# Performance work log

Measured on AMD Instinct MI355X. Metric: run time of the kernel, lower is better.

The kernel has to match this reference:

```python
import jax, jax.numpy as jnp
import numpy as np

N_ITEMS = 2000
N_STORAGE = 4094
N_LOCS = N_STORAGE + 2  # storage locations + start + end
E = 4_194_304
HID = 32


def setup_inputs() -> dict:
    rng = np.random.default_rng(0)
    etype = rng.integers(0, 3, size=E)  # 0: loc-loc, 1: item-item, 2: item-loc
    src = np.empty(E, dtype=np.int64)
    dst = np.empty(E, dtype=np.int64)
    m0, m1, m2 = (etype == 0), (etype == 1), (etype == 2)
    src[m0] = rng.integers(N_ITEMS, N_ITEMS + N_LOCS, m0.sum())
    dst[m0] = rng.integers(N_ITEMS, N_ITEMS + N_LOCS, m0.sum())
    src[m1] = rng.integers(0, N_ITEMS, m1.sum())
    dst[m1] = rng.integers(0, N_ITEMS, m1.sum())
    src[m2] = rng.integers(0, N_ITEMS, m2.sum())
    dst[m2] = rng.integers(N_ITEMS, N_ITEMS + N_STORAGE, m2.sum())
    edge_index = jnp.asarray(np.stack([src, dst]))
    edge_attr = jnp.asarray(rng.random((E, 2)).astype(np.float32))
    edge_type_mask = jnp.asarray(np.eye(3, dtype=bool)[etype])
    k1, k2 = jax.random.split(jax.random.key(0))
    W1 = jax.random.normal(k1, (3, HID), jnp.float32) * 0.5
    b1 = jnp.zeros((HID,), jnp.float32)
    W2 = jax.random.normal(k2, (HID, 1), jnp.float32) * 0.5
    b2 = jnp.zeros((1,), jnp.float32)
    return {
        "edge_index": edge_index,
        "edge_attr": edge_attr,
        "edge_type_mask": edge_type_mask,
        "n_items": N_ITEMS,
        "n_storage": N_STORAGE,
        "n_locs": N_LOCS,
        "W1": W1, "b1": b1, "W2": W2, "b2": b2,
    }


def reference(edge_index, edge_attr, edge_type_mask, n_items, n_storage, n_locs,
              W1, b1, W2, b2):
    src, dst = edge_index[0], edge_index[1]

    # --- loc-loc distance matrix: scatter masked edges into [n_locs, n_locs] ---
    ls, ld = src - n_items, dst - n_items
    v = edge_type_mask[:, 0] & (ls >= 0) & (ls < n_locs) & (ld >= 0) & (ld < n_locs)
    ls = jnp.where(v, ls, n_locs)  # invalid -> out of bounds, dropped by scatter
    ld = jnp.where(v, ld, n_locs)
    loc_mat = jnp.zeros((n_locs, n_locs), edge_attr.dtype).at[ls, ld].set(
        edge_attr[:, 0], mode="drop")

    # --- item-item sequence-count matrix: [n_items, n_items] ---
    v = edge_type_mask[:, 1] & (src >= 0) & (src < n_items) & (dst >= 0) & (dst < n_items)
    is_ = jnp.where(v, src, n_items)
    id_ = jnp.where(v, dst, n_items)
    seq_mat = jnp.zeros((n_items, n_items), edge_attr.dtype).at[is_, id_].set(
        edge_attr[:, 1], mode="drop")

    # --- item -> storage-location assignment: [n_items] int ---
    li = dst - n_items
    v = edge_type_mask[:, 2] & (src >= 0) & (src < n_items) & (li >= 0) & (li < n_storage)
    ii = jnp.where(v, src, n_items)
    item_to_loc = jnp.zeros((n_items,), jnp.int32).at[ii].set(
        jnp.where(v, li, 0).astype(jnp.int32), mode="drop")

    # --- item_item_dist = sum_{i,j: seq>0} seq_mat[i,j] * loc_mat[loc_i, loc_j] ---
    gathered = loc_mat[item_to_loc][:, item_to_loc]  # [n_items, n_items]
    item_item_dist = jnp.sum(jnp.where(seq_mat > 0, seq_mat * gathered, 0.0))

    # --- start / end depot distances (start_idx = n_storage, end_idx = n_storage+1) ---
    start_dist = jnp.sum(loc_mat[n_storage, item_to_loc]) if n_storage < n_locs else jnp.float32(0.0)
    end_dist = jnp.sum(loc_mat[item_to_loc, n_storage + 1]) if n_storage + 1 < n_locs else jnp.float32(0.0)

    comps = jnp.stack([item_item_dist, start_dist, end_dist])[None, :]  # [1, 3]
    h = jax.nn.relu(comps @ W1 + b1)
    pred = h @ W2 + b2  # [1, 1]
    return pred.squeeze()
```

## Files before the change

kernel.cpp:

```cpp
#include <hip/hip_runtime.h>

#define N_ITEMS   2000
#define N_STORAGE 4094
#define N_LOCS    4096
#define E_EDGES   4194304
#define LOCD      2048
#define NBLKB     512
#define BCAP      8192
#define SGRP      500
#define LGRP      512
#define NG        1012
#define NROWS     1013

typedef unsigned int u32;
typedef int vi4 __attribute__((ext_vector_type(4)));

__device__ __forceinline__ int wave_incl_scan(int v) {
    #pragma unroll
    for (int o = 1; o < 64; o <<= 1) {
        int u = __shfl_up(v, o);
        if ((threadIdx.x & 63) >= o) v += u;
    }
    return v;
}

__global__ __launch_bounds__(1024)
void bin_all(const int* __restrict__ src, const int* __restrict__ dst,
             u32* __restrict__ recbuf, int* __restrict__ pfx,
             int* __restrict__ slab, int* __restrict__ flags4) {
    __shared__ int lwin[N_ITEMS];
    __shared__ int cnt[NG];
    __shared__ int excl[NG];
    __shared__ int wsum[16];
    int t = threadIdx.x;
    for (int i = t; i < N_ITEMS; i += 1024) lwin[i] = -1;
    for (int i = t; i < NG; i += 1024) cnt[i] = 0;
    if (t < 32) flags4[blockIdx.x * 32 + t] = 0;
    int rel0 = t * 8;
    int base = blockIdx.x * BCAP + rel0;
    vi4 sa = __builtin_nontemporal_load((const vi4*)&src[base]);
    vi4 sb = __builtin_nontemporal_load((const vi4*)&src[base + 4]);
    vi4 da = __builtin_nontemporal_load((const vi4*)&dst[base]);
    vi4 db = __builtin_nontemporal_load((const vi4*)&dst[base + 4]);
    __syncthreads();
    int ss[8] = {sa[0], sa[1], sa[2], sa[3], sb[0], sb[1], sb[2], sb[3]};
    int dd[8] = {da[0], da[1], da[2], da[3], db[0], db[1], db[2], db[3]};
    u32 meta[8], ilcol[8];
    #pragma unroll
    for (int k = 0; k < 8; ++k) {
        int s = ss[k], d = dd[k];
        u32 m = 0xFFFFFFFFu, ic = 0;
        if ((unsigned)s < N_ITEMS) {
            if ((unsigned)d < N_ITEMS) {
                int g = s >> 2;
                m = ((u32)atomicAdd(&cnt[g], 1) << 10) | (u32)g;
                ic = ((u32)(s & 3) << 25) | ((u32)d << 13);
            } else {
                unsigned li = (unsigned)(d - N_ITEMS);
                if (li < N_STORAGE) atomicMax(&lwin[s], base + k);
            }
        } else {
            unsigned ls = (unsigned)(s - N_ITEMS), ld = (unsigned)(d - N_ITEMS);
            if (ls < N_LOCS && ld < N_LOCS) {
                int g = SGRP + (int)(ls >> 3);
                m = ((u32)atomicAdd(&cnt[g], 1) << 10) | (u32)g;
                ic = ((ls & 7u) << 25) | (ld << 13);
            }
        }
        meta[k] = m;
        ilcol[k] = ic;
    }
    __syncthreads();
    int v = (t < NG) ? cnt[t] : 0;
    int inc = wave_incl_scan(v);
    if ((t & 63) == 63) wsum[t >> 6] = inc;
    __syncthreads();
    int w = t >> 6, woff = 0;
    #pragma unroll
    for (int k = 0; k < 16; ++k) woff += (k < w) ? wsum[k] : 0;
    int ex = inc - v + woff;
    if (t < NG) {
        excl[t] = ex;
        pfx[t * NBLKB + blockIdx.x] = ex;
    }
    if (t == 0) {
        int tot = 0;
        #pragma unroll
        for (int k = 0; k < 16; ++k) tot += wsum[k];
        pfx[NG * NBLKB + blockIdx.x] = tot;
    }
    __syncthreads();
    u32* rb = recbuf + (size_t)blockIdx.x * BCAP;
    #pragma unroll
    for (int k = 0; k < 8; ++k) {
        u32 m = meta[k];
        if (m != 0xFFFFFFFFu) {
            int g = (int)(m & 1023u), rank = (int)(m >> 10);
            rb[excl[g] + rank] = ilcol[k] | (u32)(rel0 + k);
        }
    }
    for (int i = t; i < N_ITEMS; i += 1024) slab[blockIdx.x * 2048 + i] = lwin[i];
}

__global__ __launch_bounds__(1024)
void item_reduce(const int* __restrict__ slab, const int* __restrict__ dst,
                 int* __restrict__ item_loc, int* __restrict__ used_row,
                 int* __restrict__ used_col) {
    __shared__ int red[16][64];
    int t = threadIdx.x;
    int lane = t & 63, sub = t >> 6;
    int i = blockIdx.x * 64 + lane;
    int m = -1;
    for (int b = sub; b < NBLKB; b += 16)
        m = max(m, slab[b * 2048 + i]);
    red[sub][lane] = m;
    __syncthreads();
    if (sub == 0 && i < N_ITEMS) {
        #pragma unroll
        for (int k = 1; k < 16; ++k) m = max(m, red[k][lane]);
        int loc = (m >= 0) ? (dst[m] - N_ITEMS) : 0;
        item_loc[i] = loc;
        used_row[loc] = 1;
        used_col[loc] = 1;
    }
    if (blockIdx.x == 0 && t == 0) {
        used_row[N_STORAGE] = 1;
        used_col[N_STORAGE + 1] = 1;
    }
}

__global__ __launch_bounds__(1024)
void remap_fused(const int* __restrict__ used_row, const int* __restrict__ used_col,
                 const int* __restrict__ item_loc, int* __restrict__ rrow,
                 int* __restrict__ rcol, int* __restrict__ item_rr,
                 int* __restrict__ item_rc, int* __restrict__ rse) {
    __shared__ int wsA[16], wsB[16];
    int t = threadIdx.x;
    vi4 ur = *(const vi4*)&used_row[t * 4];
    vi4 uc = *(const vi4*)&used_col[t * 4];
    int sA = ur[0] + ur[1] + ur[2] + ur[3];
    int sB = uc[0] + uc[1] + uc[2] + uc[3];
    int iA = wave_incl_scan(sA);
    int iB = wave_incl_scan(sB);
    if ((t & 63) == 63) { wsA[t >> 6] = iA; wsB[t >> 6] = iB; }
    __syncthreads();
    int w = t >> 6, oA = 0, oB = 0;
    #pragma unroll
    for (int k = 0; k < 16; ++k) {
        oA += (k < w) ? wsA[k] : 0;
        oB += (k < w) ? wsB[k] : 0;
    }
    int runA = iA - sA + oA;
    int runB = iB - sB + oB;
    vi4 rr4, rc4;
    #pragma unroll
    for (int j = 0; j < 4; ++j) {
        runA += ur[j]; rr4[j] = ur[j] ? runA : 0;
        runB += uc[j]; rc4[j] = uc[j] ? runB : 0;
    }
    *(vi4*)&rrow[t * 4] = rr4;
    *(vi4*)&rcol[t * 4] = rc4;
    __syncthreads();
    for (int i = t; i < N_ITEMS; i += 1024) {
        int loc = item_loc[i];
        item_rr[i] = rrow[loc] - 1;
        item_rc[i] = rcol[loc] - 1;
    }
    if (t == 0) {
        rse[0] = rrow[N_STORAGE] - 1;
        rse[1] = rcol[N_STORAGE + 1] - 1;
    }
}

__global__ __launch_bounds__(1024)
void loc_dedup(const u32* __restrict__ recbuf, const int* __restrict__ pfx,
               const float* __restrict__ attr, const int* __restrict__ rrow,
               const int* __restrict__ rcol, float* __restrict__ locf) {
    __shared__ u32 win[8 * 2048];
    __shared__ short rcol_s[N_LOCS];
    __shared__ int rrow8[8];
    int t = threadIdx.x, g = blockIdx.x;
    if (t < 8) rrow8[t] = rrow[g * 8 + t];
    for (int i = t; i < 8 * 2048; i += 1024) win[i] = 0;
    for (int i = t; i < N_LOCS; i += 1024) rcol_s[i] = (short)rcol[i];
    __syncthreads();
    int row = SGRP + g;
    int b = t >> 1, half = t & 1;
    int s0 = pfx[row * NBLKB + b], s1 = pfx[(row + 1) * NBLKB + b];
    const u32* rb = recbuf + (size_t)b * BCAP;
    u32 kb = ((u32)b << 13) + 1;
    for (int r = s0 + half; r < s1; r += 2) {
        u32 rec = rb[r];
        int il = (int)(rec >> 25);
        if (rrow8[il] <= 0) continue;
        int rc = rcol_s[(rec >> 13) & 4095u];
        if (rc <= 0) continue;
        atomicMax(&win[il * 2048 + rc - 1], kb + (rec & 8191u));
    }
    __syncthreads();
    for (int il = 0; il < 8; ++il) {
        int cr = rrow8[il];
        if (cr <= 0) continue;
        const u32* wrow = &win[il * 2048];
        float* orow = locf + (size_t)(cr - 1) * LOCD;
        for (int i = t; i < 2048; i += 1024) {
            u32 w = wrow[i];
            orow[i] = w ? attr[2 * (int)(w - 1)] : 0.f;
        }
    }
}

__global__ __launch_bounds__(1024)
void seq_dedup(const u32* __restrict__ recbuf, const int* __restrict__ pfx,
               const float* __restrict__ attr, const float* __restrict__ locf,
               const int* __restrict__ item_rr, const int* __restrict__ item_rc,
               const int* __restrict__ rse, float* __restrict__ gpart) {
    __shared__ u32 win[4 * 2048];
    __shared__ short rcs[N_ITEMS];
    __shared__ int rrs[4];
    __shared__ float red[16][3];
    int t = threadIdx.x, g = blockIdx.x;
    for (int i = t; i < 4 * 2048; i += 1024) win[i] = 0;
    for (int i = t; i < N_ITEMS; i += 1024) rcs[i] = (short)item_rc[i];
    if (t < 4) rrs[t] = item_rr[g * 4 + t];
    __syncthreads();
    int b = t >> 1, half = t & 1;
    int s0 = pfx[g * NBLKB + b], s1 = pfx[(g + 1) * NBLKB + b];
    const u32* rb = recbuf + (size_t)b * BCAP;
    u32 kb = ((u32)b << 13) + 1;
    for (int r = s0 + half; r < s1; r += 2) {
        u32 rec = rb[r];
        int slot = (((int)(rec >> 25) & 3) << 11) | (int)((rec >> 13) & 2047u);
        atomicMax(&win[slot], kb + (rec & 8191u));
    }
    __syncthreads();
    float acc = 0.f, sd = 0.f, ed = 0.f;
    for (int i = t; i < 4 * 2048; i += 1024) {
        u32 w = win[i];
        if (w) {
            float seq = attr[2 * (int)(w - 1) + 1];
            if (seq > 0.f)
                acc += seq * locf[(size_t)rrs[i >> 11] * LOCD + (int)rcs[i & 2047]];
        }
    }
    if (t < 4) {
        sd = locf[(size_t)rse[0] * LOCD + (int)rcs[g * 4 + t]];
        ed = locf[(size_t)rrs[t] * LOCD + rse[1]];
    }
    #pragma unroll
    for (int o = 32; o > 0; o >>= 1) {
        acc += __shfl_down(acc, o);
        sd  += __shfl_down(sd, o);
        ed  += __shfl_down(ed, o);
    }
    if ((t & 63) == 0) { red[t >> 6][0] = acc; red[t >> 6][1] = sd; red[t >> 6][2] = ed; }
    __syncthreads();
    if (t == 0) {
        float a = 0.f, bb = 0.f, c = 0.f;
        #pragma unroll
        for (int k = 0; k < 16; ++k) { a += red[k][0]; bb += red[k][1]; c += red[k][2]; }
        gpart[g * 3 + 0] = a;
        gpart[g * 3 + 1] = bb;
        gpart[g * 3 + 2] = c;
    }
}

__global__ void final_mlp(const float* __restrict__ gpart, const float* __restrict__ W1,
                          const float* __restrict__ b1, const float* __restrict__ W2,
                          const float* __restrict__ b2, float* __restrict__ out) {
    __shared__ float s0[4], s1[4], s2[4];
    int t = threadIdx.x;
    float a = 0.f, b = 0.f, c = 0.f;
    for (int i = t; i < SGRP; i += 256) {
        a += gpart[i * 3 + 0];
        b += gpart[i * 3 + 1];
        c += gpart[i * 3 + 2];
    }
    #pragma unroll
    for (int o = 32; o > 0; o >>= 1) {
        a += __shfl_down(a, o);
        b += __shfl_down(b, o);
        c += __shfl_down(c, o);
    }
    if ((t & 63) == 0) { s0[t >> 6] = a; s1[t >> 6] = b; s2[t >> 6] = c; }
    __syncthreads();
    float v = 0.f;
    if (t < 32) {
        float ca = s0[0] + s0[1] + s0[2] + s0[3];
        float cb = s1[0] + s1[1] + s1[2] + s1[3];
        float cc = s2[0] + s2[1] + s2[2] + s2[3];
        float h = ca * W1[t] + cb * W1[32 + t] + cc * W1[64 + t] + b1[t];
        h = fmaxf(h, 0.f);
        v = h * W2[t];
    }
    #pragma unroll
    for (int o = 32; o > 0; o >>= 1) v += __shfl_down(v, o);
    if (t == 0) out[0] = v + b2[0];
}

extern "C" void kernel_launch(void* const* d_in, const int* in_sizes, int n_in,
                              void* d_out, int out_size, void* d_ws, size_t ws_size,
                              hipStream_t stream) {
    const int*   eidx = (const int*)d_in[0];
    const int*   src  = eidx;
    const int*   dst  = eidx + E_EDGES;
    const float* attr = (const float*)d_in[1];
    const float* W1 = (const float*)d_in[6];
    const float* b1 = (const float*)d_in[7];
    const float* W2 = (const float*)d_in[8];
    const float* b2 = (const float*)d_in[9];

    u32*   recbuf   = (u32*)d_ws;
    float* locf     = (float*)(recbuf + (size_t)NBLKB * BCAP);
    int*   used_row = (int*)(locf + (size_t)LOCD * LOCD);
    int*   used_col = used_row + N_LOCS;
    int*   rrow     = used_col + N_LOCS;
    int*   rcol     = rrow + N_LOCS;
    int*   pfx      = rcol + N_LOCS;
    int*   slab     = pfx + NROWS * NBLKB;
    int*   item_loc = slab + NBLKB * 2048;
    int*   item_rr  = item_loc + N_ITEMS;
    int*   item_rc  = item_rr + N_ITEMS;
    int*   rse      = item_rc + N_ITEMS;
    float* gpart    = (float*)(rse + 2);

    bin_all    <<<NBLKB, 1024, 0, stream>>>(src, dst, recbuf, pfx, slab, used_row);
    item_reduce<<<32, 1024, 0, stream>>>(slab, dst, item_loc, used_row, used_col);
    remap_fused<<<1, 1024, 0, stream>>>(used_row, used_col, item_loc, rrow, rcol,
                                        item_rr, item_rc, rse);
    loc_dedup  <<<LGRP, 1024, 0, stream>>>(recbuf, pfx, attr, rrow, rcol, locf);
    seq_dedup  <<<SGRP, 1024, 0, stream>>>(recbuf, pfx, attr, locf,
                                           item_rr, item_rc, rse, gpart);
    final_mlp  <<<1, 256, 0, stream>>>(gpart, W1, b1, W2, b2, (float*)d_out);
}
```

Before: 88.52 us.

## Halve binning blocks and carry seq attribute inside 64-bit records

The binning kernel now runs 256 blocks of 16384 edges each and streams the edge attributes alongside src/dst. Item-item records become 64-bit values that carry the seq float, so seq_dedup does its atomicMax on 64-bit keys and no longer gathers attr at random. Seq and loc records go to separate buffers with their own prefix arrays, and the dedup kernels use 4 threads per source block instead of 2. In exchange, bin_all reads every attribute and has fewer blocks, which lowers its parallelism, and the 64-bit LDS atomics and larger record buffers add cost.

```diff
diff --git a/kernel.cpp b/kernel.cpp
--- a/kernel.cpp
+++ b/kernel.cpp
@@ -5,15 +5,16 @@
 #define N_LOCS    4096
 #define E_EDGES   4194304
 #define LOCD      2048
-#define NBLKB     512
-#define BCAP      8192
+#define NBLKB     256
+#define BCAP      16384
 #define SGRP      500
 #define LGRP      512
 #define NG        1012
-#define NROWS     1013
-
+
+typedef unsigned long long u64;
 typedef unsigned int u32;
-typedef int vi4 __attribute__((ext_vector_type(4)));
+typedef int   vi4 __attribute__((ext_vector_type(4)));
+typedef float vf4 __attribute__((ext_vector_type(4)));
 
 __device__ __forceinline__ int wave_incl_scan(int v) {
     #pragma unroll
@@ -26,77 +27,99 @@
 
 __global__ __launch_bounds__(1024)
 void bin_all(const int* __restrict__ src, const int* __restrict__ dst,
-             u32* __restrict__ recbuf, int* __restrict__ pfx,
+             const float* __restrict__ attr, u64* __restrict__ seqrec,
+             u32* __restrict__ locrec, int* __restrict__ pfxS, int* __restrict__ pfxL,
              int* __restrict__ slab, int* __restrict__ flags4) {
     __shared__ int lwin[N_ITEMS];
     __shared__ int cnt[NG];
-    __shared__ int excl[NG];
+    __shared__ int exclS[SGRP];
+    __shared__ int exclL[LGRP];
     __shared__ int wsum[16];
     int t = threadIdx.x;
     for (int i = t; i < N_ITEMS; i += 1024) lwin[i] = -1;
     for (int i = t; i < NG; i += 1024) cnt[i] = 0;
-    if (t < 32) flags4[blockIdx.x * 32 + t] = 0;
-    int rel0 = t * 8;
-    int base = blockIdx.x * BCAP + rel0;
-    vi4 sa = __builtin_nontemporal_load((const vi4*)&src[base]);
-    vi4 sb = __builtin_nontemporal_load((const vi4*)&src[base + 4]);
-    vi4 da = __builtin_nontemporal_load((const vi4*)&dst[base]);
-    vi4 db = __builtin_nontemporal_load((const vi4*)&dst[base + 4]);
-    __syncthreads();
-    int ss[8] = {sa[0], sa[1], sa[2], sa[3], sb[0], sb[1], sb[2], sb[3]};
-    int dd[8] = {da[0], da[1], da[2], da[3], db[0], db[1], db[2], db[3]};
-    u32 meta[8], ilcol[8];
-    #pragma unroll
-    for (int k = 0; k < 8; ++k) {
-        int s = ss[k], d = dd[k];
-        u32 m = 0xFFFFFFFFu, ic = 0;
-        if ((unsigned)s < N_ITEMS) {
-            if ((unsigned)d < N_ITEMS) {
-                int g = s >> 2;
-                m = ((u32)atomicAdd(&cnt[g], 1) << 10) | (u32)g;
-                ic = ((u32)(s & 3) << 25) | ((u32)d << 13);
+    if (t < 64) flags4[blockIdx.x * 64 + t] = 0;
+    __syncthreads();
+
+    u32 meta[16], aux[16], val[16];
+    #pragma unroll
+    for (int r = 0; r < 2; ++r) {
+        int rel0 = r * 8192 + t * 8;
+        int base = blockIdx.x * BCAP + rel0;
+        vi4 sa = __builtin_nontemporal_load((const vi4*)&src[base]);
+        vi4 sb = __builtin_nontemporal_load((const vi4*)&src[base + 4]);
+        vi4 da = __builtin_nontemporal_load((const vi4*)&dst[base]);
+        vi4 db = __builtin_nontemporal_load((const vi4*)&dst[base + 4]);
+        vf4 a0 = __builtin_nontemporal_load((const vf4*)&attr[base * 2]);
+        vf4 a1 = __builtin_nontemporal_load((const vf4*)&attr[base * 2 + 4]);
+        vf4 a2 = __builtin_nontemporal_load((const vf4*)&attr[base * 2 + 8]);
+        vf4 a3 = __builtin_nontemporal_load((const vf4*)&attr[base * 2 + 12]);
+        int ss[8] = {sa[0], sa[1], sa[2], sa[3], sb[0], sb[1], sb[2], sb[3]};
+        int dd[8] = {da[0], da[1], da[2], da[3], db[0], db[1], db[2], db[3]};
+        float v1[8] = {a0[1], a0[3], a1[1], a1[3], a2[1], a2[3], a3[1], a3[3]};
+        #pragma unroll
+        for (int k = 0; k < 8; ++k) {
+            int e = r * 8 + k;
+            int s = ss[k], d = dd[k];
+            u32 m = 0xFFFFFFFFu, ic = 0, vv = 0;
+            if ((unsigned)s < N_ITEMS) {
+                if ((unsigned)d < N_ITEMS) {
+                    int g = s >> 2;
+                    m = ((u32)atomicAdd(&cnt[g], 1) << 10) | (u32)g;
+                    ic = ((u32)(s & 3) << 25) | ((u32)d << 14) | (u32)(rel0 + k);
+                    vv = __float_as_uint(v1[k]);
+                } else {
+                    unsigned li = (unsigned)(d - N_ITEMS);
+                    if (li < N_STORAGE) atomicMax(&lwin[s], base + k);
+                }
             } else {
-                unsigned li = (unsigned)(d - N_ITEMS);
-                if (li < N_STORAGE) atomicMax(&lwin[s], base + k);
+                unsigned ls = (unsigned)(s - N_ITEMS), ld = (unsigned)(d - N_ITEMS);
+                if (ls < N_LOCS && ld < N_LOCS) {
+                    int g = SGRP + (int)(ls >> 3);
+                    m = ((u32)atomicAdd(&cnt[g], 1) << 10) | (u32)g;
+                    ic = ((ls & 7u) << 26) | (ld << 14) | (u32)(rel0 + k);
+                }
             }
-        } else {
-            unsigned ls = (unsigned)(s - N_ITEMS), ld = (unsigned)(d - N_ITEMS);
-            if (ls < N_LOCS && ld < N_LOCS) {
-                int g = SGRP + (int)(ls >> 3);
-                m = ((u32)atomicAdd(&cnt[g], 1) << 10) | (u32)g;
-                ic = ((ls & 7u) << 25) | (ld << 13);
-            }
+            meta[e] = m;
+            aux[e] = ic;
+            val[e] = vv;
         }
-        meta[k] = m;
-        ilcol[k] = ic;
-    }
-    __syncthreads();
-    int v = (t < NG) ? cnt[t] : 0;
+    }
+    __syncthreads();
+    int v;
+    if (t < 512) v = (t < SGRP) ? cnt[t] : 0;
+    else         v = cnt[t - 12];
     int inc = wave_incl_scan(v);
     if ((t & 63) == 63) wsum[t >> 6] = inc;
     __syncthreads();
-    int w = t >> 6, woff = 0;
-    #pragma unroll
-    for (int k = 0; k < 16; ++k) woff += (k < w) ? wsum[k] : 0;
+    int w = t >> 6, lo = (t < 512) ? 0 : 8, woff = 0;
+    #pragma unroll
+    for (int k = 0; k < 16; ++k) woff += (k >= lo && k < w) ? wsum[k] : 0;
     int ex = inc - v + woff;
-    if (t < NG) {
-        excl[t] = ex;
-        pfx[t * NBLKB + blockIdx.x] = ex;
+    if (t < SGRP) {
+        exclS[t] = ex;
+        pfxS[t * NBLKB + blockIdx.x] = ex;
+    } else if (t >= 512) {
+        exclL[t - 512] = ex;
+        pfxL[(t - 512) * NBLKB + blockIdx.x] = ex;
     }
     if (t == 0) {
-        int tot = 0;
+        int t0 = 0, t1 = 0;
         #pragma unroll
-        for (int k = 0; k < 16; ++k) tot += wsum[k];
-        pfx[NG * NBLKB + blockIdx.x] = tot;
-    }
-    __syncthreads();
-    u32* rb = recbuf + (size_t)blockIdx.x * BCAP;
-    #pragma unroll
-    for (int k = 0; k < 8; ++k) {
-        u32 m = meta[k];
+        for (int k = 0; k < 8; ++k) { t0 += wsum[k]; t1 += wsum[k + 8]; }
+        pfxS[SGRP * NBLKB + blockIdx.x] = t0;
+        pfxL[LGRP * NBLKB + blockIdx.x] = t1;
+    }
+    __syncthreads();
+    u64* srb = seqrec + (size_t)blockIdx.x * BCAP;
+    u32* lrb = locrec + (size_t)blockIdx.x * BCAP;
+    #pragma unroll
+    for (int e = 0; e < 16; ++e) {
+        u32 m = meta[e];
         if (m != 0xFFFFFFFFu) {
             int g = (int)(m & 1023u), rank = (int)(m >> 10);
-            rb[excl[g] + rank] = ilcol[k] | (u32)(rel0 + k);
+            if (g < SGRP) srb[exclS[g] + rank] = ((u64)aux[e] << 32) | (u64)val[e];
+            else          lrb[exclL[g - SGRP] + rank] = aux[e];
         }
     }
     for (int i = t; i < N_ITEMS; i += 1024) slab[blockIdx.x * 2048 + i] = lwin[i];
@@ -173,7 +196,7 @@
 }
 
 __global__ __launch_bounds__(1024)
-void loc_dedup(const u32* __restrict__ recbuf, const int* __restrict__ pfx,
+void loc_dedup(const u32* __restrict__ locrec, const int* __restrict__ pfxL,
                const float* __restrict__ attr, const int* __restrict__ rrow,
                const int* __restrict__ rcol, float* __restrict__ locf) {
     __shared__ u32 win[8 * 2048];
@@ -184,18 +207,17 @@
     for (int i = t; i < 8 * 2048; i += 1024) win[i] = 0;
     for (int i = t; i < N_LOCS; i += 1024) rcol_s[i] = (short)rcol[i];
     __syncthreads();
-    int row = SGRP + g;
-    int b = t >> 1, half = t & 1;
-    int s0 = pfx[row * NBLKB + b], s1 = pfx[(row + 1) * NBLKB + b];
-    const u32* rb = recbuf + (size_t)b * BCAP;
-    u32 kb = ((u32)b << 13) + 1;
-    for (int r = s0 + half; r < s1; r += 2) {
+    int b = t >> 2, q = t & 3;
+    int s0 = pfxL[g * NBLKB + b], s1 = pfxL[(g + 1) * NBLKB + b];
+    const u32* rb = locrec + (size_t)b * BCAP;
+    u32 kb = ((u32)b << 14) + 1;
+    for (int r = s0 + q; r < s1; r += 4) {
         u32 rec = rb[r];
-        int il = (int)(rec >> 25);
+        int il = (int)(rec >> 26);
         if (rrow8[il] <= 0) continue;
-        int rc = rcol_s[(rec >> 13) & 4095u];
+        int rc = rcol_s[(rec >> 14) & 4095u];
         if (rc <= 0) continue;
-        atomicMax(&win[il * 2048 + rc - 1], kb + (rec & 8191u));
+        atomicMax(&win[il * 2048 + rc - 1], kb + (rec & 16383u));
     }
     __syncthreads();
     for (int il = 0; il < 8; ++il) {
@@ -211,11 +233,11 @@
 }
 
 __global__ __launch_bounds__(1024)
-void seq_dedup(const u32* __restrict__ recbuf, const int* __restrict__ pfx,
-               const float* __restrict__ attr, const float* __restrict__ locf,
-               const int* __restrict__ item_rr, const int* __restrict__ item_rc,
-               const int* __restrict__ rse, float* __restrict__ gpart) {
-    __shared__ u32 win[4 * 2048];
+void seq_dedup(const u64* __restrict__ seqrec, const int* __restrict__ pfxS,
+               const float* __restrict__ locf, const int* __restrict__ item_rr,
+               const int* __restrict__ item_rc, const int* __restrict__ rse,
+               float* __restrict__ gpart) {
+    __shared__ u64 win[4 * 2048];
     __shared__ short rcs[N_ITEMS];
     __shared__ int rrs[4];
     __shared__ float red[16][3];
@@ -224,21 +246,22 @@
     for (int i = t; i < N_ITEMS; i += 1024) rcs[i] = (short)item_rc[i];
     if (t < 4) rrs[t] = item_rr[g * 4 + t];
     __syncthreads();
-    int b = t >> 1, half = t & 1;
-    int s0 = pfx[g * NBLKB + b], s1 = pfx[(g + 1) * NBLKB + b];
-    const u32* rb = recbuf + (size_t)b * BCAP;
-    u32 kb = ((u32)b << 13) + 1;
-    for (int r = s0 + half; r < s1; r += 2) {
-        u32 rec = rb[r];
-        int slot = (((int)(rec >> 25) & 3) << 11) | (int)((rec >> 13) & 2047u);
-        atomicMax(&win[slot], kb + (rec & 8191u));
+    int b = t >> 2, q = t & 3;
+    int s0 = pfxS[g * NBLKB + b], s1 = pfxS[(g + 1) * NBLKB + b];
+    const u64* rb = seqrec + (size_t)b * BCAP;
+    u64 kb = ((u64)((u32)b << 14) + 1) << 32;
+    for (int r = s0 + q; r < s1; r += 4) {
+        u64 rec = rb[r];
+        u32 ax = (u32)(rec >> 32);
+        int slot = (((int)(ax >> 25) & 3) << 11) | (int)((ax >> 14) & 2047u);
+        atomicMax(&win[slot], kb + ((u64)(ax & 16383u) << 32) + (rec & 0xFFFFFFFFull));
     }
     __syncthreads();
     float acc = 0.f, sd = 0.f, ed = 0.f;
     for (int i = t; i < 4 * 2048; i += 1024) {
-        u32 w = win[i];
+        u64 w = win[i];
         if (w) {
-            float seq = attr[2 * (int)(w - 1) + 1];
+            float seq = __uint_as_float((u32)(w & 0xFFFFFFFFull));
             if (seq > 0.f)
                 acc += seq * locf[(size_t)rrs[i >> 11] * LOCD + (int)rcs[i & 2047]];
         }
@@ -310,26 +333,29 @@
     const float* W2 = (const float*)d_in[8];
     const float* b2 = (const float*)d_in[9];
 
-    u32*   recbuf   = (u32*)d_ws;
-    float* locf     = (float*)(recbuf + (size_t)NBLKB * BCAP);
+    u64*   seqrec   = (u64*)d_ws;
+    u32*   locrec   = (u32*)(seqrec + (size_t)NBLKB * BCAP);
+    float* locf     = (float*)(locrec + (size_t)NBLKB * BCAP);
     int*   used_row = (int*)(locf + (size_t)LOCD * LOCD);
     int*   used_col = used_row + N_LOCS;
     int*   rrow     = used_col + N_LOCS;
     int*   rcol     = rrow + N_LOCS;
-    int*   pfx      = rcol + N_LOCS;
-    int*   slab     = pfx + NROWS * NBLKB;
+    int*   pfxS     = rcol + N_LOCS;
+    int*   pfxL     = pfxS + (SGRP + 1) * NBLKB;
+    int*   slab     = pfxL + (LGRP + 1) * NBLKB;
     int*   item_loc = slab + NBLKB * 2048;
     int*   item_rr  = item_loc + N_ITEMS;
     int*   item_rc  = item_rr + N_ITEMS;
     int*   rse      = item_rc + N_ITEMS;
     float* gpart    = (float*)(rse + 2);
 
-    bin_all    <<<NBLKB, 1024, 0, stream>>>(src, dst, recbuf, pfx, slab, used_row);
+    bin_all    <<<NBLKB, 1024, 0, stream>>>(src, dst, attr, seqrec, locrec,
+                                            pfxS, pfxL, slab, used_row);
     item_reduce<<<32, 1024, 0, stream>>>(slab, dst, item_loc, used_row, used_col);
     remap_fused<<<1, 1024, 0, stream>>>(used_row, used_col, item_loc, rrow, rcol,
                                         item_rr, item_rc, rse);
-    loc_dedup  <<<LGRP, 1024, 0, stream>>>(recbuf, pfx, attr, rrow, rcol, locf);
-    seq_dedup  <<<SGRP, 1024, 0, stream>>>(recbuf, pfx, attr, locf,
+    loc_dedup  <<<LGRP, 1024, 0, stream>>>(locrec, pfxL, attr, rrow, rcol, locf);
+    seq_dedup  <<<SGRP, 1024, 0, stream>>>(seqrec, pfxS, locf,
                                            item_rr, item_rc, rse, gpart);
     final_mlp  <<<1, 256, 0, stream>>>(gpart, W1, b1, W2, b2, (float*)d_out);
 }
```

Result: faster. 85.23 us (-3.7%).
